# Kernel optimization log

Measured on AMD Instinct MI355X. Metric: run time of the kernel, lower is better.

Reference implementation:

```python
import jax, jax.numpy as jnp
import numpy as np

HEADS = 4
F_OUT = 64
NEG_SLOPE = 0.2


def setup_inputs() -> dict:
    key = jax.random.key(0)
    k1, k2, k3, k4 = jax.random.split(key, 4)
    N, F_IN = 4096, 256
    x = jax.random.normal(k1, (N, F_IN), dtype=jnp.float32)
    adj = jax.random.randint(k2, (N, N), 0, 2, dtype=jnp.int32)
    # nn.Linear stores weight [out, in]; we store transposed [in, out] for x @ W
    W = jax.random.normal(k3, (F_IN, F_OUT * HEADS), dtype=jnp.float32) * (1.0 / np.sqrt(F_IN))
    a = jax.random.normal(k4, (2 * F_OUT, 1), dtype=jnp.float32) * 0.1
    return {"x": x, "adj": adj, "W": W, "a": a}


def reference(x, adj, W, a):
    N = x.shape[0]
    h = (x @ W).reshape(N, HEADS, F_OUT)              # [N, H, F]
    # matmul(cat(h_i, h_j), a) == h_i @ a1 + h_j @ a2 (exact, avoids O(N^2*2F) h_cat)
    a1 = a[:F_OUT, 0]
    a2 = a[F_OUT:, 0]
    e_i = jnp.einsum('nhf,f->nh', h, a1)              # [N, H]
    e_j = jnp.einsum('nhf,f->nh', h, a2)              # [N, H]
    e = e_i[:, None, :] + e_j[None, :, :]             # [N, N, H]
    e = jnp.where(e > 0, e, NEG_SLOPE * e)            # LeakyReLU(0.2)
    e = jnp.where(adj[:, :, None] == 0, -jnp.inf, e)
    attention = jax.nn.softmax(e, axis=1)             # softmax over source nodes j
    h_prime = jnp.einsum('ijh,jhf->ihf', attention, h)  # [N, H, F]
    return h_prime.mean(axis=1)                       # heads > 1 -> mean over heads
```

## Files before the change

### kernel.cpp

```cpp
#include <hip/hip_runtime.h>

#define N     4096
#define FIN   256
#define CC    256
#define HEADS 4
#define FOUT  64
#define XPITCH 266

typedef __attribute__((ext_vector_type(8))) short bf16x8;
typedef __attribute__((ext_vector_type(4))) float f32x4;

__device__ inline short f2bf(float f) {
    unsigned u = __builtin_bit_cast(unsigned, f);
    unsigned r = u + 0x7fffu + ((u >> 16) & 1u);
    return (short)(r >> 16);
}

__global__ __launch_bounds__(512) void gat_k1a(const float* __restrict__ x,
                                               const float* __restrict__ W,
                                               const float* __restrict__ a,
                                               short* __restrict__ hF,
                                               float2* __restrict__ e1f,
                                               float2* __restrict__ e2f) {
    __shared__ __align__(16) short xs[64][XPITCH];
    __shared__ __align__(16) short wts[64][XPITCH];
    __shared__ __align__(16) short hbuf[64][74];
    const int t    = threadIdx.x;
    const int bid  = blockIdx.x;
    const int lane = t & 63;
    const int w    = t >> 6;

    const int hd = bid >> 6;
    const int n0 = (bid & 63) * 64;
    const int c0 = hd * 64;

    {
        const float4* xsrc = (const float4*)(x + (size_t)n0 * FIN);
        #pragma unroll
        for (int it = 0; it < 8; ++it) {
            const int fi = it * 512 + t;
            const float4 v = xsrc[fi];
            short4 o;
            o.x = f2bf(v.x); o.y = f2bf(v.y); o.z = f2bf(v.z); o.w = f2bf(v.w);
            *(short4*)&xs[fi >> 6][(fi & 63) * 4] = o;
        }
    }
    {
        const int c  = t & 63;
        const int k4 = (t >> 6) * 4;
        #pragma unroll
        for (int it = 0; it < 8; ++it) {
            const int k = it * 32 + k4;
            short4 pk;
            pk.x = f2bf(W[(k + 0) * CC + c0 + c]);
            pk.y = f2bf(W[(k + 1) * CC + c0 + c]);
            pk.z = f2bf(W[(k + 2) * CC + c0 + c]);
            pk.w = f2bf(W[(k + 3) * CC + c0 + c]);
            *(short4*)&wts[c][k] = pk;
        }
    }
    __syncthreads();

    const int m = lane & 15;
    const int q = lane >> 4;

    if (w < 4) {
        f32x4 acc[4];
        #pragma unroll
        for (int ct = 0; ct < 4; ++ct) acc[ct] = (f32x4){0.f, 0.f, 0.f, 0.f};

        #pragma unroll
        for (int ks = 0; ks < 8; ++ks) {
            const bf16x8 af = *(const bf16x8*)&xs[w * 16 + m][ks * 32 + q * 8];
            #pragma unroll
            for (int ct = 0; ct < 4; ++ct) {
                const bf16x8 bf_ = *(const bf16x8*)&wts[ct * 16 + m][ks * 32 + q * 8];
                acc[ct] = __builtin_amdgcn_mfma_f32_16x16x32_bf16(af, bf_, acc[ct], 0, 0, 0);
            }
        }

        const float a1v[4] = {a[m], a[16 + m], a[32 + m], a[48 + m]};
        const float a2v[4] = {a[64 + m], a[80 + m], a[96 + m], a[112 + m]};
        #pragma unroll
        for (int r = 0; r < 4; ++r) {
            float s1 = 0.f, s2 = 0.f;
            #pragma unroll
            for (int ct = 0; ct < 4; ++ct) {
                s1 = fmaf(acc[ct][r], a1v[ct], s1);
                s2 = fmaf(acc[ct][r], a2v[ct], s2);
            }
            #pragma unroll
            for (int sh = 1; sh < 16; sh <<= 1) {
                s1 += __shfl_xor(s1, sh, 64);
                s2 += __shfl_xor(s2, sh, 64);
            }
            if (m == 0) {
                const int n = n0 + w * 16 + q * 4 + r;
                e1f[(size_t)hd * N + n] = make_float2(__expf(s1), __expf(0.2f * s1));
                e2f[(size_t)hd * N + n] = make_float2(__expf(s2), __expf(0.2f * s2));
            }
        }

        #pragma unroll
        for (int ct = 0; ct < 4; ++ct)
            #pragma unroll
            for (int r = 0; r < 4; ++r)
                hbuf[ct * 16 + m][w * 16 + q * 4 + r] = f2bf(acc[ct][r]);
    }
    __syncthreads();

    {
        const int lp = t & 63;
        const int ft = (t >> 6) & 3;
        const int c2 = t >> 8;
        const int mm = lp & 15;
        const int qq = lp >> 4;
        const bf16x8 hv = *(const bf16x8*)&hbuf[ft * 16 + mm][c2 * 32 + qq * 8];
        const size_t jc = (size_t)(n0 >> 5) + c2;
        *(bf16x8*)(hF + ((((size_t)hd * 128 + jc) * 4 + ft) * 64 + lp) * 8) = hv;
    }
}

__global__ __launch_bounds__(256) void gat_k1b(const int* __restrict__ adj,
                                               unsigned* __restrict__ adjb) {
    const int t    = threadIdx.x;
    const int lane = t & 63;
    const int w    = t >> 6;
    const int row  = blockIdx.x * 2 + (w >> 1);
    const int half = w & 1;
    const int4* arow4 = (const int4*)(adj + (size_t)row * N) + half * 512;
    unsigned*   drow  = adjb + (size_t)row * 128 + half * 64;

    int4 ca[8];
    #pragma unroll
    for (int k = 0; k < 8; ++k)
        ca[k] = arow4[k * 64 + lane];
    #pragma unroll
    for (int k = 0; k < 8; ++k) {
        const int4 v = ca[k];
        unsigned n = (v.x != 0 ? 1u : 0u) | (v.y != 0 ? 2u : 0u) |
                     (v.z != 0 ? 4u : 0u) | (v.w != 0 ? 8u : 0u);
        unsigned b  = n   | ((unsigned)__shfl_xor((int)n,   1, 64) << 4);
        unsigned hw = b   | ((unsigned)__shfl_xor((int)b,   2, 64) << 8);
        unsigned d  = hw  | ((unsigned)__shfl_xor((int)hw,  4, 64) << 16);
        if ((lane & 7) == 0) drow[k * 8 + (lane >> 3)] = d;
    }
}

__global__ __launch_bounds__(512, 4) void gat_k2b(const short* __restrict__ hF,
                                                  const unsigned* __restrict__ adjb,
                                                  const float2* __restrict__ e1f,
                                                  const float2* __restrict__ e2f,
                                                  float* __restrict__ num,
                                                  float* __restrict__ Zp) {
    __shared__ __align__(16) short    hstage[2][4096];
    __shared__ __align__(16) float    e2s[2048];
    __shared__ __align__(16) unsigned adjl[128 * 36];
    const int t    = threadIdx.x;
    const int lane = t & 63;
    const int g    = t >> 6;
    const int bid  = blockIdx.x;
    const int xcd  = bid & 7;
    const int idx  = bid >> 3;
    const int hd   = idx & 3;
    const int jc   = (idx >> 2) & 3;
    const int it   = xcd | ((idx >> 4) << 3);
    const int i0   = it * 128;
    const int j0   = jc * 1024;
    const int m    = lane & 15;
    const int q    = lane >> 4;
    const int slice = hd * 4 + jc;

    ((float4*)e2s)[t] = ((const float4*)(e2f + (size_t)hd * N + j0))[t];
    {
        const int row = t >> 2, part = t & 3;
        const uint4* src = (const uint4*)(adjb + (size_t)(i0 + row) * 128 + jc * 32 + part * 8);
        uint4* dst = (uint4*)(adjl + row * 36 + part * 8);
        dst[0] = src[0];
        dst[1] = src[1];
    }
    const uint4* gsrc = (const uint4*)(hF + ((size_t)hd * 128 + jc * 32) * 2048);
    ((uint4*)hstage[0])[t] = gsrc[t];
    __syncthreads();

    const int    rowi = i0 + g * 16 + m;
    const float2 E1r  = e1f[(size_t)hd * N + rowi];
    const float  E1x  = E1r.x;
    const float  E1y  = E1r.y;

    f32x4 acc[4];
    #pragma unroll
    for (int ft = 0; ft < 4; ++ft) acc[ft] = (f32x4){0.f, 0.f, 0.f, 0.f};
    float zacc = 0.f;

    const unsigned char* ab = ((const unsigned char*)adjl) + (g * 16 + m) * 144 + q;

    int cur = 0;
    #pragma unroll 2
    for (int mac = 0; mac < 16; ++mac) {
        const uint4 v = gsrc[(size_t)((mac + 1) & 15) * 512 + t];

        const short* hb = &hstage[cur][0];
        #pragma unroll
        for (int s = 0; s < 2; ++s) {
            const int jloc = mac * 64 + s * 32 + q * 8;
            const bf16x8 b0 = *(const bf16x8*)(hb + s * 2048 + 0 * 512 + lane * 8);
            const bf16x8 b1 = *(const bf16x8*)(hb + s * 2048 + 1 * 512 + lane * 8);
            const bf16x8 b2 = *(const bf16x8*)(hb + s * 2048 + 2 * 512 + lane * 8);
            const bf16x8 b3 = *(const bf16x8*)(hb + s * 2048 + 3 * 512 + lane * 8);
            const float4* ev = (const float4*)&e2s[2 * jloc];
            const float4 d0 = ev[0], d1 = ev[1], d2 = ev[2], d3 = ev[3];
            const unsigned bits = (unsigned)ab[(mac * 2 + s) * 4];

            const float ep[8] = {d0.x, d0.z, d1.x, d1.z, d2.x, d2.z, d3.x, d3.z};
            const float en[8] = {d0.y, d0.w, d1.y, d1.w, d2.y, d2.w, d3.y, d3.w};

            bf16x8 af;
            #pragma unroll
            for (int jj = 0; jj < 8; ++jj) {
                const unsigned msk = (unsigned)(((int)(bits << (31 - jj))) >> 31);
                float wv = fmaxf(E1x * ep[jj], E1y * en[jj]);
                wv = __builtin_bit_cast(float, __builtin_bit_cast(unsigned, wv) & msk);
                zacc += wv;
                af[jj] = f2bf(wv);
            }

            acc[0] = __builtin_amdgcn_mfma_f32_16x16x32_bf16(af, b0, acc[0], 0, 0, 0);
            acc[1] = __builtin_amdgcn_mfma_f32_16x16x32_bf16(af, b1, acc[1], 0, 0, 0);
            acc[2] = __builtin_amdgcn_mfma_f32_16x16x32_bf16(af, b2, acc[2], 0, 0, 0);
            acc[3] = __builtin_amdgcn_mfma_f32_16x16x32_bf16(af, b3, acc[3], 0, 0, 0);
        }

        if (mac < 15) {
            ((uint4*)hstage[cur ^ 1])[t] = v;
            __syncthreads();
            cur ^= 1;
        }
    }

    zacc += __shfl_xor(zacc, 16, 64);
    zacc += __shfl_xor(zacc, 32, 64);
    if (lane < 16)
        Zp[(size_t)slice * N + i0 + g * 16 + lane] = zacc;

    {
        float* nrow = num + ((size_t)slice * N + i0 + g * 16) * FOUT;
        #pragma unroll
        for (int ft = 0; ft < 4; ++ft)
            #pragma unroll
            for (int r = 0; r < 4; ++r)
                nrow[(q * 4 + r) * FOUT + ft * 16 + m] = acc[ft][r];
    }
}

__global__ __launch_bounds__(256) void gat_k3(const float* __restrict__ num,
                                              const float* __restrict__ Zp,
                                              float* __restrict__ out) {
    const int g4 = blockIdx.x * 256 + threadIdx.x;
    const int i  = g4 >> 4;
    const int fo = (g4 & 15) * 4;
    float4 r = make_float4(0.f, 0.f, 0.f, 0.f);
    #pragma unroll
    for (int hd = 0; hd < 4; ++hd) {
        float4 s = make_float4(0.f, 0.f, 0.f, 0.f);
        float  z = 0.f;
        #pragma unroll
        for (int jc = 0; jc < 4; ++jc) {
            const int sl = hd * 4 + jc;
            const float4 v = *(const float4*)(num + ((size_t)sl * N + i) * FOUT + fo);
            s.x += v.x; s.y += v.y; s.z += v.z; s.w += v.w;
            z += Zp[(size_t)sl * N + i];
        }
        const float inv = 1.f / z;
        r.x += s.x * inv; r.y += s.y * inv; r.z += s.z * inv; r.w += s.w * inv;
    }
    r.x *= 0.25f; r.y *= 0.25f; r.z *= 0.25f; r.w *= 0.25f;
    *(float4*)(out + (size_t)i * FOUT + fo) = r;
}

extern "C" void kernel_launch(void* const* d_in, const int* in_sizes, int n_in,
                              void* d_out, int out_size, void* d_ws, size_t ws_size,
                              hipStream_t stream) {
    const float* x   = (const float*)d_in[0];
    const int*   adj = (const int*)d_in[1];
    const float* W   = (const float*)d_in[2];
    const float* a   = (const float*)d_in[3];
    float* out = (float*)d_out;

    short*    hF   = (short*)d_ws;
    float2*   e1f  = (float2*)(hF + (size_t)HEADS * FOUT * N);
    float2*   e2f  = e1f + (size_t)HEADS * N;
    unsigned* adjb = (unsigned*)(e2f + (size_t)HEADS * N);
    float*    num  = (float*)(adjb + (size_t)N * 128);
    float*    Zp   = num + (size_t)16 * N * FOUT;

    gat_k1a<<<256, 512, 0, stream>>>(x, W, a, hF, e1f, e2f);
    gat_k1b<<<2048, 256, 0, stream>>>(adj, adjb);
    gat_k2b<<<512, 512, 0, stream>>>(hF, adjb, e1f, e2f, num, Zp);
    gat_k3<<<256, 256, 0, stream>>>(num, Zp, out);
}
```

Before: 136.0 us.

## Use packed bf16 conversion, packed muls, mask lookup table and MFMA row-sum

Replaces the software bf16 rounding with the hardware v_cvt_pk_bf16_f32 instruction, computes attention weights with packed f32 multiplies, and applies the adjacency mask via a shared-memory lookup table on the packed bf16 values. The softmax denominator is now accumulated through an extra MFMA against a ones vector, replacing the scalar VALU accumulation and shuffles. This cuts VALU work in the hot loop of the aggregation kernel. In exchange it adds one MFMA per step and sums bf16-rounded weights, which differs slightly from the previous fp32 sum.

```diff
diff --git a/kernel.cpp b/kernel.cpp
--- a/kernel.cpp
+++ b/kernel.cpp
@@ -9,11 +9,17 @@
 
 typedef __attribute__((ext_vector_type(8))) short bf16x8;
 typedef __attribute__((ext_vector_type(4))) float f32x4;
-
-__device__ inline short f2bf(float f) {
-    unsigned u = __builtin_bit_cast(unsigned, f);
-    unsigned r = u + 0x7fffu + ((u >> 16) & 1u);
-    return (short)(r >> 16);
+typedef __attribute__((ext_vector_type(2))) float f32x2;
+
+__device__ inline unsigned cvtpk(float lo, float hi) {
+    unsigned r;
+    asm("v_cvt_pk_bf16_f32 %0, %1, %2" : "=v"(r) : "v"(lo), "v"(hi));
+    return r;
+}
+__device__ inline f32x2 pkmul(f32x2 a, f32x2 b) {
+    f32x2 r;
+    asm("v_pk_mul_f32 %0, %1, %2" : "=v"(r) : "v"(a), "v"(b));
+    return r;
 }
 
 __global__ __launch_bounds__(512) void gat_k1a(const float* __restrict__ x,
@@ -40,9 +46,10 @@
         for (int it = 0; it < 8; ++it) {
             const int fi = it * 512 + t;
             const float4 v = xsrc[fi];
-            short4 o;
-            o.x = f2bf(v.x); o.y = f2bf(v.y); o.z = f2bf(v.z); o.w = f2bf(v.w);
-            *(short4*)&xs[fi >> 6][(fi & 63) * 4] = o;
+            uint2 o;
+            o.x = cvtpk(v.x, v.y);
+            o.y = cvtpk(v.z, v.w);
+            *(uint2*)&xs[fi >> 6][(fi & 63) * 4] = o;
         }
     }
     {
@@ -51,12 +58,14 @@
         #pragma unroll
         for (int it = 0; it < 8; ++it) {
             const int k = it * 32 + k4;
-            short4 pk;
-            pk.x = f2bf(W[(k + 0) * CC + c0 + c]);
-            pk.y = f2bf(W[(k + 1) * CC + c0 + c]);
-            pk.z = f2bf(W[(k + 2) * CC + c0 + c]);
-            pk.w = f2bf(W[(k + 3) * CC + c0 + c]);
-            *(short4*)&wts[c][k] = pk;
+            const float w0 = W[(k + 0) * CC + c0 + c];
+            const float w1 = W[(k + 1) * CC + c0 + c];
+            const float w2 = W[(k + 2) * CC + c0 + c];
+            const float w3 = W[(k + 3) * CC + c0 + c];
+            uint2 o;
+            o.x = cvtpk(w0, w1);
+            o.y = cvtpk(w2, w3);
+            *(uint2*)&wts[c][k] = o;
         }
     }
     __syncthreads();
@@ -102,10 +111,13 @@
         }
 
         #pragma unroll
-        for (int ct = 0; ct < 4; ++ct)
-            #pragma unroll
-            for (int r = 0; r < 4; ++r)
-                hbuf[ct * 16 + m][w * 16 + q * 4 + r] = f2bf(acc[ct][r]);
+        for (int ct = 0; ct < 4; ++ct) {
+            const unsigned lo = cvtpk(acc[ct][0], acc[ct][1]);
+            const unsigned hi = cvtpk(acc[ct][2], acc[ct][3]);
+            unsigned* hp = (unsigned*)&hbuf[ct * 16 + m][w * 16 + q * 4];
+            hp[0] = lo;
+            hp[1] = hi;
+        }
     }
     __syncthreads();
 
@@ -156,6 +168,7 @@
     __shared__ __align__(16) short    hstage[2][4096];
     __shared__ __align__(16) float    e2s[2048];
     __shared__ __align__(16) unsigned adjl[128 * 36];
+    __shared__ __align__(16) uint4    mtab[256];
     const int t    = threadIdx.x;
     const int lane = t & 63;
     const int g    = t >> 6;
@@ -179,19 +192,31 @@
         dst[0] = src[0];
         dst[1] = src[1];
     }
+    if (t < 256) {
+        const unsigned b = t;
+        uint4 e;
+        e.x = ((b & 1u)   ? 0xFFFFu : 0u) | ((b & 2u)   ? 0xFFFF0000u : 0u);
+        e.y = ((b & 4u)   ? 0xFFFFu : 0u) | ((b & 8u)   ? 0xFFFF0000u : 0u);
+        e.z = ((b & 16u)  ? 0xFFFFu : 0u) | ((b & 32u)  ? 0xFFFF0000u : 0u);
+        e.w = ((b & 64u)  ? 0xFFFFu : 0u) | ((b & 128u) ? 0xFFFF0000u : 0u);
+        mtab[b] = e;
+    }
     const uint4* gsrc = (const uint4*)(hF + ((size_t)hd * 128 + jc * 32) * 2048);
     ((uint4*)hstage[0])[t] = gsrc[t];
     __syncthreads();
 
     const int    rowi = i0 + g * 16 + m;
     const float2 E1r  = e1f[(size_t)hd * N + rowi];
-    const float  E1x  = E1r.x;
-    const float  E1y  = E1r.y;
+    const f32x2  E1pk = (f32x2){E1r.x, E1r.y};
+
+    bf16x8 onesb;
+    #pragma unroll
+    for (int e = 0; e < 8; ++e) onesb[e] = (short)0x3F80;
 
     f32x4 acc[4];
     #pragma unroll
     for (int ft = 0; ft < 4; ++ft) acc[ft] = (f32x4){0.f, 0.f, 0.f, 0.f};
-    float zacc = 0.f;
+    f32x4 accz = (f32x4){0.f, 0.f, 0.f, 0.f};
 
     const unsigned char* ab = ((const unsigned char*)adjl) + (g * 16 + m) * 144 + q;
 
@@ -199,6 +224,11 @@
     #pragma unroll 2
     for (int mac = 0; mac < 16; ++mac) {
         const uint4 v = gsrc[(size_t)((mac + 1) & 15) * 512 + t];
+
+        const unsigned bits0 = (unsigned)ab[(mac * 2 + 0) * 4];
+        const unsigned bits1 = (unsigned)ab[(mac * 2 + 1) * 4];
+        const uint4 mk0 = mtab[bits0];
+        const uint4 mk1 = mtab[bits1];
 
         const short* hb = &hstage[cur][0];
         #pragma unroll
@@ -210,25 +240,29 @@
             const bf16x8 b3 = *(const bf16x8*)(hb + s * 2048 + 3 * 512 + lane * 8);
             const float4* ev = (const float4*)&e2s[2 * jloc];
             const float4 d0 = ev[0], d1 = ev[1], d2 = ev[2], d3 = ev[3];
-            const unsigned bits = (unsigned)ab[(mac * 2 + s) * 4];
-
-            const float ep[8] = {d0.x, d0.z, d1.x, d1.z, d2.x, d2.z, d3.x, d3.z};
-            const float en[8] = {d0.y, d0.w, d1.y, d1.w, d2.y, d2.w, d3.y, d3.w};
-
-            bf16x8 af;
-            #pragma unroll
-            for (int jj = 0; jj < 8; ++jj) {
-                const unsigned msk = (unsigned)(((int)(bits << (31 - jj))) >> 31);
-                float wv = fmaxf(E1x * ep[jj], E1y * en[jj]);
-                wv = __builtin_bit_cast(float, __builtin_bit_cast(unsigned, wv) & msk);
-                zacc += wv;
-                af[jj] = f2bf(wv);
-            }
+            const uint4 mk = s ? mk1 : mk0;
+
+            const f32x2 p0 = pkmul(E1pk, (f32x2){d0.x, d0.y});
+            const f32x2 p1 = pkmul(E1pk, (f32x2){d0.z, d0.w});
+            const f32x2 p2 = pkmul(E1pk, (f32x2){d1.x, d1.y});
+            const f32x2 p3 = pkmul(E1pk, (f32x2){d1.z, d1.w});
+            const f32x2 p4 = pkmul(E1pk, (f32x2){d2.x, d2.y});
+            const f32x2 p5 = pkmul(E1pk, (f32x2){d2.z, d2.w});
+            const f32x2 p6 = pkmul(E1pk, (f32x2){d3.x, d3.y});
+            const f32x2 p7 = pkmul(E1pk, (f32x2){d3.z, d3.w});
+
+            uint4 afu;
+            afu.x = cvtpk(fmaxf(p0[0], p0[1]), fmaxf(p1[0], p1[1])) & mk.x;
+            afu.y = cvtpk(fmaxf(p2[0], p2[1]), fmaxf(p3[0], p3[1])) & mk.y;
+            afu.z = cvtpk(fmaxf(p4[0], p4[1]), fmaxf(p5[0], p5[1])) & mk.z;
+            afu.w = cvtpk(fmaxf(p6[0], p6[1]), fmaxf(p7[0], p7[1])) & mk.w;
+            const bf16x8 af = __builtin_bit_cast(bf16x8, afu);
 
             acc[0] = __builtin_amdgcn_mfma_f32_16x16x32_bf16(af, b0, acc[0], 0, 0, 0);
             acc[1] = __builtin_amdgcn_mfma_f32_16x16x32_bf16(af, b1, acc[1], 0, 0, 0);
             acc[2] = __builtin_amdgcn_mfma_f32_16x16x32_bf16(af, b2, acc[2], 0, 0, 0);
             acc[3] = __builtin_amdgcn_mfma_f32_16x16x32_bf16(af, b3, acc[3], 0, 0, 0);
+            accz   = __builtin_amdgcn_mfma_f32_16x16x32_bf16(af, onesb, accz, 0, 0, 0);
         }
 
         if (mac < 15) {
@@ -238,10 +272,11 @@
         }
     }
 
-    zacc += __shfl_xor(zacc, 16, 64);
-    zacc += __shfl_xor(zacc, 32, 64);
-    if (lane < 16)
-        Zp[(size_t)slice * N + i0 + g * 16 + lane] = zacc;
+    if (m == 0) {
+        #pragma unroll
+        for (int r = 0; r < 4; ++r)
+            Zp[(size_t)slice * N + i0 + g * 16 + q * 4 + r] = accz[r];
+    }
 
     {
         float* nrow = num + ((size_t)slice * N + i0 + g * 16) * FOUT;
```

Result: faster. 132.6 us (-2.5%).
